# Optimization experiments

Measured on AMD Instinct MI355X. Metric: run time of the kernel, lower is better.

The kernel has to match this reference:

```python
import jax, jax.numpy as jnp
import numpy as np

THRESHOLD = 0.5
NEG_POS_RATIO = 3
VARIANCE = (0.1, 0.2)


def point_form(p):
    # center-form (cx,cy,w,h) -> corner-form (xmin,ymin,xmax,ymax)
    return jnp.concatenate([p[:, :2] - p[:, 2:] / 2, p[:, :2] + p[:, 2:] / 2], axis=-1)


def jaccard(a, b):
    # a: [N,4] corner boxes, b: [P,4] corner boxes -> IoU [N,P]
    lt = jnp.maximum(a[:, None, :2], b[None, :, :2])
    rb = jnp.minimum(a[:, None, 2:], b[None, :, 2:])
    wh = jnp.clip(rb - lt, 0.0)
    inter = wh[..., 0] * wh[..., 1]
    area_a = ((a[:, 2] - a[:, 0]) * (a[:, 3] - a[:, 1]))[:, None]
    area_b = ((b[:, 2] - b[:, 0]) * (b[:, 3] - b[:, 1]))[None, :]
    return inter / (area_a + area_b - inter)


def encode(matched, priors_cf):
    # matched: [P,4] corner GT boxes, priors_cf: [P,4] center-form priors
    g_cxcy = (matched[:, :2] + matched[:, 2:]) / 2 - priors_cf[:, :2]
    g_cxcy = g_cxcy / (VARIANCE[0] * priors_cf[:, 2:])
    g_wh = jnp.log((matched[:, 2:] - matched[:, :2]) / priors_cf[:, 2:]) / VARIANCE[1]
    return jnp.concatenate([g_cxcy, g_wh], axis=-1)  # [P,4]


def match_one(truths, labels, priors_cf):
    # truths: [N,4], labels: [N], priors_cf: [P,4]
    n_obj = truths.shape[0]
    overlaps = jaccard(truths, point_form(priors_cf))          # [N,P]
    best_prior_idx = jnp.argmax(overlaps, axis=1)              # [N] best prior per GT
    best_truth_overlap = jnp.max(overlaps, axis=0)             # [P]
    best_truth_idx = jnp.argmax(overlaps, axis=0)              # [P] best GT per prior
    # ensure every GT keeps its best prior
    best_truth_overlap = best_truth_overlap.at[best_prior_idx].set(2.0)
    best_truth_idx = best_truth_idx.at[best_prior_idx].set(jnp.arange(n_obj))
    matched = truths[best_truth_idx]                           # [P,4]
    conf = jnp.where(best_truth_overlap < THRESHOLD, 0, labels[best_truth_idx] + 1)
    return encode(matched, priors_cf), conf.astype(jnp.int32)


def setup_inputs() -> dict:
    key = jax.random.key(0)
    k1, k2, k3, k4, k5, k6, k7 = jax.random.split(key, 7)
    B, P, C, NOBJ = 64, 24564, 21, 32
    loc_data = jax.random.normal(k1, (B, P, 4), jnp.float32)
    conf_data = jax.random.normal(k2, (B, P, C), jnp.float32)
    p_cxcy = jax.random.uniform(k3, (P, 2), jnp.float32, 0.05, 0.95)
    p_wh = jax.random.uniform(k4, (P, 2), jnp.float32, 0.02, 0.4)
    priors = jnp.concatenate([p_cxcy, p_wh], axis=-1)          # center-form
    t_cxcy = jax.random.uniform(k5, (B, NOBJ, 2), jnp.float32, 0.2, 0.8)
    t_wh = jax.random.uniform(k6, (B, NOBJ, 2), jnp.float32, 0.05, 0.3)
    targets_boxes = jnp.concatenate([t_cxcy - t_wh / 2, t_cxcy + t_wh / 2], axis=-1)
    targets_labels = jax.random.randint(k7, (B, NOBJ), 0, C - 1)  # 0..19, +1 in match
    return {
        "loc_data": loc_data,
        "conf_data": conf_data,
        "priors": priors,
        "targets_boxes": targets_boxes,
        "targets_labels": targets_labels,
    }


def reference(loc_data, conf_data, priors, targets_boxes, targets_labels):
    B, P, C = conf_data.shape
    # targets/priors are detached in the original (.data)
    loc_t, conf_t = jax.vmap(match_one, in_axes=(0, 0, None))(
        jax.lax.stop_gradient(targets_boxes), targets_labels,
        jax.lax.stop_gradient(priors))                          # [B,P,4], [B,P]

    pos = conf_t > 0                                            # [B,P]
    num_pos = jnp.sum(pos, axis=1)                              # [B]

    # localization: smooth L1 on positives, summed
    diff = loc_data - loc_t
    ad = jnp.abs(diff)
    sl1 = jnp.where(ad < 1.0, 0.5 * diff * diff, ad - 0.5)      # [B,P,4]
    loss_l = jnp.sum(sl1 * pos[..., None].astype(sl1.dtype))

    # confidence cross-entropy per prior: lse(x) - x[target]
    lse = jax.nn.logsumexp(conf_data, axis=-1)                  # [B,P]
    gathered = jnp.take_along_axis(conf_data, conf_t[..., None], axis=-1)[..., 0]
    ce_all = lse - gathered                                     # [B,P]

    # hard negative mining: rank negatives by loss, keep top 3*num_pos
    loss_mine = jnp.where(pos, 0.0, ce_all)
    order = jnp.argsort(-loss_mine, axis=1)
    idx_rank = jnp.argsort(order, axis=1)                       # rank of each prior
    num_neg = jnp.clip(NEG_POS_RATIO * num_pos, 0, P - 1)       # [B]
    neg = idx_rank < num_neg[:, None]

    mask = jnp.logical_or(pos, neg)
    loss_c = jnp.sum(ce_all * mask.astype(ce_all.dtype))

    N = jnp.maximum(jnp.sum(num_pos), 1).astype(loss_l.dtype)
    return jnp.stack([loss_l / N, loss_c / N])
```

## Files before the change

kernel.cpp:

```cpp
#include <hip/hip_runtime.h>
#include <stdint.h>

#define THRESH 0.5f
#define VAR0 0.1f
#define VAR1 0.2f
#define SEL_MAXV 32

__global__ __launch_bounds__(256) void fused_kernel(
    const float* __restrict__ loc_data, const float* __restrict__ conf_data,
    const float* __restrict__ priors, const float* __restrict__ tboxes,
    const int* __restrict__ labels,
    unsigned long long* __restrict__ part_best,
    float* __restrict__ loss_mine,
    float* __restrict__ ll_part, float* __restrict__ pc_part,
    int* __restrict__ np_part, unsigned int* __restrict__ done_ctr,
    int P, int C, int NOBJ, int NBLK)
{
#pragma clang fp contract(off)
    extern __shared__ char smem[];
    float* siou = (float*)smem;
    unsigned long long (*sp)[17] =
        (unsigned long long (*)[17])(smem + 16 * 257 * 4);
    float* confs = (float*)smem;
    __shared__ float4 tr[32];
    __shared__ float ta[32];

    const int b = blockIdx.y, bx = blockIdx.x, tid = threadIdx.x;
    const int p = bx * 256 + tid;
    if (b == 0 && bx == 0 && tid == 0) *done_ctr = 0;
    if (tid < NOBJ) {
        float4 t = ((const float4*)tboxes)[(size_t)b * NOBJ + tid];
        tr[tid] = t;
        ta[tid] = (t.z - t.x) * (t.w - t.y);
    }
    __syncthreads();

    const bool valid = (p < P);
    float ax = 0.f, ay = 0.f, bxx = 0.f, byy = 0.f, area_p = 0.f;
    if (valid) {
        float4 pr = ((const float4*)priors)[p];
        ax = pr.x - pr.z * 0.5f;
        ay = pr.y - pr.w * 0.5f;
        bxx = pr.x + pr.z * 0.5f;
        byy = pr.y + pr.w * 0.5f;
        area_p = (bxx - ax) * (byy - ay);
    }

    float bestv = -1.0f;
    int bestn = 0;
    for (int n0 = 0; n0 < NOBJ; n0 += 16) {
        const int jmax = min(16, NOBJ - n0);
        for (int j = 0; j < jmax; ++j) {
            float4 t = tr[n0 + j];
            float iou = -1.0f;
            if (valid) {
                float ltx = fmaxf(t.x, ax), lty = fmaxf(t.y, ay);
                float rbx = fminf(t.z, bxx), rby = fminf(t.w, byy);
                float w = rbx - ltx; if (w < 0.f) w = 0.f;
                float h = rby - lty; if (h < 0.f) h = 0.f;
                float inter = w * h;
                float denom = (ta[n0 + j] + area_p) - inter;
                iou = inter * __builtin_amdgcn_rcpf(denom);
                if (iou > bestv) { bestv = iou; bestn = n0 + j; }
            }
            siou[j * 257 + tid] = iou;
        }
        __syncthreads();
        {
            const int n2 = tid & 15, c = tid >> 4;
            if (n2 < jmax) {
                float bv = -1.0f;
                int bs = 0;
                const int base = n2 * 257 + c * 16;
                for (int j2 = 0; j2 < 16; ++j2) {
                    float v = siou[base + j2];
                    if (v > bv) { bv = v; bs = c * 16 + j2; }
                }
                unsigned long long pk = 0ULL;
                if (bv >= 0.f) {
                    unsigned int pp = (unsigned int)(bx * 256 + bs);
                    pk = (((unsigned long long)__float_as_uint(bv)) << 32) |
                         (unsigned long long)(0xFFFFFFFFu - pp);
                }
                sp[n0 + n2][c] = pk;
            }
        }
        __syncthreads();
    }
    if (tid < NOBJ) {
        unsigned long long best = 0ULL;
        for (int c = 0; c < 16; ++c) {
            unsigned long long v = sp[tid][c];
            if (v > best) best = v;
        }
        part_best[((size_t)b * NBLK + bx) * NOBJ + tid] = best;
    }
    __syncthreads();

    const int p0 = bx * 256;
    const int rows = min(256, P - p0);
    const int nflt = rows * C;
    const float* src = conf_data + ((size_t)b * P + p0) * C;
    if ((((uintptr_t)src) & 15) == 0) {
        const int n4 = nflt >> 2;
        const float4* src4 = (const float4*)src;
        for (int i = tid; i < n4; i += 256) ((float4*)confs)[i] = src4[i];
        for (int i = (n4 << 2) + tid; i < nflt; i += 256) confs[i] = src[i];
    } else {
        for (int i = tid; i < nflt; i += 256) confs[i] = src[i];
    }
    __syncthreads();

    float ll = 0.f, pc = 0.f;
    int np = 0;
    if (tid < rows) {
        const size_t g = (size_t)b * P + p;
        int conf_t = (bestv < THRESH) ? 0 : labels[b * NOBJ + bestn] + 1;

        const float* row = confs + tid * C;
        float s = 0.f;
        for (int j = 0; j < C; ++j) s += __expf(row[j]);
        float ce = __logf(s) - row[conf_t];

        bool pos = (conf_t > 0);
        loss_mine[g] = pos ? 0.f : ce;
        if (pos) {
            np = 1;
            pc = ce;
            float4 t = tr[bestn];
            float4 pr = ((const float4*)priors)[p];
            float gcx = ((t.x + t.z) * 0.5f - pr.x) / (VAR0 * pr.z);
            float gcy = ((t.y + t.w) * 0.5f - pr.y) / (VAR0 * pr.w);
            float gw  = __logf((t.z - t.x) / pr.z) / VAR1;
            float gh  = __logf((t.w - t.y) / pr.w) / VAR1;
            float4 ld = ((const float4*)loc_data)[g];
            float d, a;
            d = ld.x - gcx; a = fabsf(d); ll += (a < 1.f) ? 0.5f * d * d : a - 0.5f;
            d = ld.y - gcy; a = fabsf(d); ll += (a < 1.f) ? 0.5f * d * d : a - 0.5f;
            d = ld.z - gw;  a = fabsf(d); ll += (a < 1.f) ? 0.5f * d * d : a - 0.5f;
            d = ld.w - gh;  a = fabsf(d); ll += (a < 1.f) ? 0.5f * d * d : a - 0.5f;
        }
    }

    for (int off = 32; off; off >>= 1) {
        ll += __shfl_down(ll, off, 64);
        pc += __shfl_down(pc, off, 64);
        np += __shfl_down(np, off, 64);
    }
    __shared__ float sll[4], spc[4];
    __shared__ int snp[4];
    const int lane = tid & 63, wid = tid >> 6;
    if (lane == 0) { sll[wid] = ll; spc[wid] = pc; snp[wid] = np; }
    __syncthreads();
    if (tid == 0) {
        size_t slot = (size_t)b * NBLK + bx;
        ll_part[slot] = sll[0] + sll[1] + sll[2] + sll[3];
        pc_part[slot] = spc[0] + spc[1] + spc[2] + spc[3];
        np_part[slot] = snp[0] + snp[1] + snp[2] + snp[3];
    }
}

__global__ __launch_bounds__(1024) void selectcf_kernel(
    const float* __restrict__ loc_data, const float* __restrict__ conf_data,
    const float* __restrict__ priors, const float* __restrict__ tboxes,
    const int* __restrict__ labels,
    const unsigned long long* __restrict__ part_best,
    float* __restrict__ loss_mine,
    const float* __restrict__ ll_part, const float* __restrict__ pc_part,
    const int* __restrict__ np_part,
    double* __restrict__ neg, double* __restrict__ dll_b,
    double* __restrict__ dpc_b, int* __restrict__ npos_b,
    unsigned int* __restrict__ done_ctr, float* __restrict__ out,
    int P, int C, int NOBJ, int NBLK, int B, int ratio)
{
#pragma clang fp contract(off)
    const int b = blockIdx.x;
    const int tid = threadIdx.x;
    const int lane = tid & 63, wid = tid >> 6;

    __shared__ float4 tr[32];
    __shared__ unsigned long long sp2[32][17];
    __shared__ unsigned long long bb[32];
    __shared__ int2 centry[32];
    __shared__ double sdll[32], sdpc[32];
    __shared__ int cnt_s, snp_s, snp_corr;
    __shared__ unsigned int hist[16][257];
    __shared__ unsigned int merged[256];
    __shared__ unsigned int sh_sel, sh_k;
    __shared__ double sd[16];
    __shared__ unsigned int sc[16];
    __shared__ double negv_s;
    __shared__ int is_last_s;

    if (tid == 0) { cnt_s = 0; snp_s = 0; snp_corr = 0; negv_s = 0.0; }
    if (tid < NOBJ) tr[tid] = ((const float4*)tboxes)[(size_t)b * NOBJ + tid];
    __syncthreads();

    if (tid < NBLK) atomicAdd(&snp_s, np_part[b * NBLK + tid]);

    {
        const int n = tid & 31, c = tid >> 5;
        if (tid < 512 && n < NOBJ) {
            unsigned long long best = 0ULL;
            for (int j = c; j < NBLK; j += 16) {
                unsigned long long v = part_best[((size_t)b * NBLK + j) * NOBJ + n];
                if (v > best) best = v;
            }
            sp2[n][c] = best;
        }
    }
    __syncthreads();
    if (tid < NOBJ) {
        unsigned long long best = 0ULL;
        for (int c = 0; c < 16; ++c) {
            unsigned long long v = sp2[tid][c];
            if (v > best) best = v;
        }
        bb[tid] = best;
    }
    __syncthreads();

    if (tid == 0) {
        int cnt = 0;
        for (int n = 0; n < NOBJ; ++n) {
            int pidx = (int)(0xFFFFFFFFu - (unsigned int)(bb[n] & 0xFFFFFFFFu));
            int f = -1;
            for (int j = 0; j < cnt; ++j)
                if (centry[j].x == pidx) f = j;
            if (f >= 0) centry[f].y = n;
            else { centry[cnt].x = pidx; centry[cnt].y = n; ++cnt; }
        }
        cnt_s = cnt;
    }
    __syncthreads();

    if (tid < cnt_s) {
        const int pidx = centry[tid].x;
        const int n = centry[tid].y;
        float4 pr = ((const float4*)priors)[pidx];
        float ax = pr.x - pr.z * 0.5f;
        float ay = pr.y - pr.w * 0.5f;
        float bxx = pr.x + pr.z * 0.5f;
        float byy = pr.y + pr.w * 0.5f;
        float area_p = (bxx - ax) * (byy - ay);
        float bestv = -1.0f;
        int bestn = 0;
        for (int nn = 0; nn < NOBJ; ++nn) {
            float4 t = tr[nn];
            float ltx = fmaxf(t.x, ax), lty = fmaxf(t.y, ay);
            float rbx = fminf(t.z, bxx), rby = fminf(t.w, byy);
            float w = rbx - ltx; if (w < 0.f) w = 0.f;
            float h = rby - lty; if (h < 0.f) h = 0.f;
            float inter = w * h;
            float att = (t.z - t.x) * (t.w - t.y);
            float denom = (att + area_p) - inter;
            float iou = inter * __builtin_amdgcn_rcpf(denom);
            if (iou > bestv) { bestv = iou; bestn = nn; }
        }
        const float* row = conf_data + ((size_t)b * P + pidx) * C;
        float s = 0.f;
        for (int j = 0; j < C; ++j) s += __expf(row[j]);
        float lse = __logf(s);

        int old_conf = (bestv < THRESH) ? 0 : labels[b * NOBJ + bestn] + 1;
        int new_conf = labels[b * NOBJ + n] + 1;
        bool old_pos = (old_conf > 0);

        double dpc = old_pos ? ((double)row[old_conf] - (double)row[new_conf])
                             : (double)(lse - row[new_conf]);

        const size_t g = (size_t)b * P + pidx;
        float4 ld = ((const float4*)loc_data)[g];
        float sl1_new, sl1_old = 0.f;
        {
            float4 t = tr[n];
            float gcx = ((t.x + t.z) * 0.5f - pr.x) / (VAR0 * pr.z);
            float gcy = ((t.y + t.w) * 0.5f - pr.y) / (VAR0 * pr.w);
            float gw  = __logf((t.z - t.x) / pr.z) / VAR1;
            float gh  = __logf((t.w - t.y) / pr.w) / VAR1;
            float ll = 0.f, d, a;
            d = ld.x - gcx; a = fabsf(d); ll += (a < 1.f) ? 0.5f * d * d : a - 0.5f;
            d = ld.y - gcy; a = fabsf(d); ll += (a < 1.f) ? 0.5f * d * d : a - 0.5f;
            d = ld.z - gw;  a = fabsf(d); ll += (a < 1.f) ? 0.5f * d * d : a - 0.5f;
            d = ld.w - gh;  a = fabsf(d); ll += (a < 1.f) ? 0.5f * d * d : a - 0.5f;
            sl1_new = ll;
        }
        if (old_pos) {
            float4 t = tr[bestn];
            float gcx = ((t.x + t.z) * 0.5f - pr.x) / (VAR0 * pr.z);
            float gcy = ((t.y + t.w) * 0.5f - pr.y) / (VAR0 * pr.w);
            float gw  = __logf((t.z - t.x) / pr.z) / VAR1;
            float gh  = __logf((t.w - t.y) / pr.w) / VAR1;
            float ll = 0.f, d, a;
            d = ld.x - gcx; a = fabsf(d); ll += (a < 1.f) ? 0.5f * d * d : a - 0.5f;
            d = ld.y - gcy; a = fabsf(d); ll += (a < 1.f) ? 0.5f * d * d : a - 0.5f;
            d = ld.z - gw;  a = fabsf(d); ll += (a < 1.f) ? 0.5f * d * d : a - 0.5f;
            d = ld.w - gh;  a = fabsf(d); ll += (a < 1.f) ? 0.5f * d * d : a - 0.5f;
            sl1_old = ll;
        }
        sdll[tid] = (double)sl1_new - (double)sl1_old;
        sdpc[tid] = dpc;
        if (!old_pos) {
            atomicAdd(&snp_corr, 1);
            loss_mine[g] = 0.f;
        }
    }
    __syncthreads();

    int k = ratio * (snp_s + snp_corr);
    if (k > P - 1) k = P - 1;

    if (k > 0) {
        const float* fvals = loss_mine + (size_t)b * P;
        unsigned int vreg[SEL_MAXV];
#pragma unroll
        for (int j = 0; j < SEL_MAXV; ++j) {
            int i = tid + (j << 10);
            vreg[j] = (i < P) ? __float_as_uint(fvals[i]) : 0u;
        }
        unsigned int prefix = 0, mask = 0;
        unsigned int kk = (unsigned int)k;
        for (int shift = 24; shift >= 0; shift -= 8) {
            for (int t = tid; t < 16 * 257; t += 1024) (&hist[0][0])[t] = 0;
            __syncthreads();
            unsigned int* h = hist[wid];
#pragma unroll
            for (int j = 0; j < SEL_MAXV; ++j) {
                int i = tid + (j << 10);
                unsigned int v = vreg[j];
                if (i < P && (v & mask) == prefix)
                    atomicAdd(&h[(v >> shift) & 255u], 1u);
            }
            __syncthreads();
            if (tid < 256) {
                unsigned int s = 0;
                for (int w = 0; w < 16; ++w) s += hist[w][tid];
                merged[tid] = s;
            }
            __syncthreads();
            if (wid == 0) {
                unsigned int h0 = merged[4 * lane], h1 = merged[4 * lane + 1];
                unsigned int h2 = merged[4 * lane + 2], h3 = merged[4 * lane + 3];
                unsigned int s3 = h3, s2 = h2 + s3, s1 = h1 + s2, s0 = h0 + s1;
                unsigned int t = s0;
                unsigned int T = t;
                for (int off = 1; off < 64; off <<= 1) {
                    unsigned int o = __shfl_down(T, off, 64);
                    if (lane + off < 64) T += o;
                }
                unsigned int A = T - t;
                unsigned int S0 = A + s0, S1 = A + s1, S2 = A + s2, S3 = A + s3, S4 = A;
                if (S0 >= kk && S1 < kk) { sh_sel = 4 * lane + 0; sh_k = kk - S1; }
                if (S1 >= kk && S2 < kk) { sh_sel = 4 * lane + 1; sh_k = kk - S2; }
                if (S2 >= kk && S3 < kk) { sh_sel = 4 * lane + 2; sh_k = kk - S3; }
                if (S3 >= kk && S4 < kk) { sh_sel = 4 * lane + 3; sh_k = kk - S4; }
            }
            __syncthreads();
            prefix |= sh_sel << shift;
            mask |= 0xFFu << shift;
            kk = sh_k;
        }
        const float T = __uint_as_float(prefix);

        double sum = 0.0;
        unsigned int cnt = 0;
#pragma unroll
        for (int j = 0; j < SEL_MAXV; ++j) {
            int i = tid + (j << 10);
            if (i < P) {
                float v = __uint_as_float(vreg[j]);
                if (v > T) { sum += (double)v; cnt++; }
            }
        }
        for (int off = 32; off; off >>= 1) {
            sum += __shfl_down(sum, off, 64);
            cnt += __shfl_down(cnt, off, 64);
        }
        if (lane == 0) { sd[wid] = sum; sc[wid] = cnt; }
        __syncthreads();
        if (tid == 0) {
            double S = 0.0;
            unsigned int Cn = 0;
            for (int w = 0; w < 16; ++w) { S += sd[w]; Cn += sc[w]; }
            negv_s = S + (double)((unsigned int)k - Cn) * (double)T;
        }
    }
    __syncthreads();

    if (tid == 0) {
        double DL = 0.0, DP = 0.0;
        for (int j = 0; j < cnt_s; ++j) { DL += sdll[j]; DP += sdpc[j]; }
        neg[b] = negv_s;
        dll_b[b] = DL;
        dpc_b[b] = DP;
        npos_b[b] = snp_s + snp_corr;
        __threadfence();
        unsigned int old = atomicAdd(done_ctr, 1u);
        is_last_s = (old == (unsigned int)B - 1) ? 1 : 0;
    }
    __syncthreads();
    if (!is_last_s) return;
    __threadfence();

    double LL = 0.0, PC = 0.0, NG = 0.0;
    long long NP = 0;
    const int NPART = B * NBLK;
    for (int i = tid; i < NPART; i += 1024) {
        LL += (double)ll_part[i];
        PC += (double)pc_part[i];
    }
    for (int i = tid; i < B; i += 1024) {
        NG += neg[i];
        LL += dll_b[i];
        PC += dpc_b[i];
        NP += (long long)npos_b[i];
    }
    for (int off = 32; off; off >>= 1) {
        LL += __shfl_down(LL, off, 64);
        PC += __shfl_down(PC, off, 64);
        NG += __shfl_down(NG, off, 64);
        NP += __shfl_down(NP, off, 64);
    }
    __shared__ double fll[16], fpc[16], fng[16];
    __shared__ long long fnp[16];
    if (lane == 0) { fll[wid] = LL; fpc[wid] = PC; fng[wid] = NG; fnp[wid] = NP; }
    __syncthreads();
    if (tid == 0) {
        double L = 0.0, Pc = 0.0, Ng = 0.0;
        long long Np = 0;
        for (int w = 0; w < 16; ++w) { L += fll[w]; Pc += fpc[w]; Ng += fng[w]; Np += fnp[w]; }
        if (Np < 1) Np = 1;
        double N = (double)Np;
        out[0] = (float)(L / N);
        out[1] = (float)((Pc + Ng) / N);
    }
}

extern "C" void kernel_launch(void* const* d_in, const int* in_sizes, int n_in,
                              void* d_out, int out_size, void* d_ws, size_t ws_size,
                              hipStream_t stream)
{
    const float* loc_data  = (const float*)d_in[0];
    const float* conf_data = (const float*)d_in[1];
    const float* priors    = (const float*)d_in[2];
    const float* tboxes    = (const float*)d_in[3];
    const int*   tlabels   = (const int*)d_in[4];

    const int P = in_sizes[2] / 4;
    const int B = (int)((long long)in_sizes[0] / ((long long)P * 4));
    const int C = (int)((long long)in_sizes[1] / ((long long)B * P));
    const int NOBJ = in_sizes[4] / B;
    const int NBLK = (P + 255) / 256;

    char* ws = (char*)d_ws;
    size_t off = 0;
    unsigned int* done_ctr = (unsigned int*)(ws + off);  off += 256;
    double* neg = (double*)(ws + off);                   off += (size_t)B * 8;
    off = (off + 255) & ~(size_t)255;
    double* dll_b = (double*)(ws + off);                 off += (size_t)B * 8;
    off = (off + 255) & ~(size_t)255;
    double* dpc_b = (double*)(ws + off);                 off += (size_t)B * 8;
    off = (off + 255) & ~(size_t)255;
    int* npos_b = (int*)(ws + off);                      off += (size_t)B * 4;
    off = (off + 255) & ~(size_t)255;
    float* ll_part = (float*)(ws + off);                 off += (size_t)B * NBLK * 4;
    off = (off + 255) & ~(size_t)255;
    float* pc_part = (float*)(ws + off);                 off += (size_t)B * NBLK * 4;
    off = (off + 255) & ~(size_t)255;
    int* np_part = (int*)(ws + off);                     off += (size_t)B * NBLK * 4;
    off = (off + 255) & ~(size_t)255;
    unsigned long long* part_best = (unsigned long long*)(ws + off);
    off += (size_t)B * NBLK * NOBJ * 8;
    off = (off + 255) & ~(size_t)255;
    float* loss_mine = (float*)(ws + off);

    size_t smem_match = 16 * 257 * 4 + 32 * 17 * 8;
    size_t smem_conf = (size_t)256 * C * 4;
    size_t smem = smem_match > smem_conf ? smem_match : smem_conf;

    dim3 grid(NBLK, B);
    fused_kernel<<<grid, 256, smem, stream>>>(
        loc_data, conf_data, priors, tboxes, tlabels,
        part_best, loss_mine, ll_part, pc_part, np_part, done_ctr,
        P, C, NOBJ, NBLK);
    selectcf_kernel<<<B, 1024, 0, stream>>>(
        loc_data, conf_data, priors, tboxes, tlabels,
        part_best, loss_mine, ll_part, pc_part, np_part,
        neg, dll_b, dpc_b, npos_b, done_ctr, (float*)d_out,
        P, C, NOBJ, NBLK, B, 3);
}
```

Baseline: 306.0 us.

## Load conf rows directly into registers and shrink shared memory in fused kernel

Drops the shared-memory staging of the 256x21 conf tile. Each thread now prefetches its own 21-float row into registers at kernel start, so the load overlaps the IoU matching phase. Shared memory is cut to static arrays (the per-block best packing is split into a float value and a byte index) and launch bounds ask for 8 blocks per CU, aiming for higher occupancy. GT boxes are read from global memory instead of LDS, and the per-thread row loads are strided and unaligned, which may coalesce worse than the old cooperative float4 copy.

Result: faster. 290.9 us (-4.9%).

```diff
diff --git a/kernel.cpp b/kernel.cpp
--- a/kernel.cpp
+++ b/kernel.cpp
@@ -6,7 +6,9 @@
 #define VAR1 0.2f
 #define SEL_MAXV 32
 
-__global__ __launch_bounds__(256) void fused_kernel(
+typedef float f4u __attribute__((ext_vector_type(4), aligned(4)));
+
+__global__ __launch_bounds__(256, 8) void fused_kernel(
     const float* __restrict__ loc_data, const float* __restrict__ conf_data,
     const float* __restrict__ priors, const float* __restrict__ tboxes,
     const int* __restrict__ labels,
@@ -17,20 +19,34 @@
     int P, int C, int NOBJ, int NBLK)
 {
 #pragma clang fp contract(off)
-    extern __shared__ char smem[];
-    float* siou = (float*)smem;
-    unsigned long long (*sp)[17] =
-        (unsigned long long (*)[17])(smem + 16 * 257 * 4);
-    float* confs = (float*)smem;
-    __shared__ float4 tr[32];
+    __shared__ float siou[16 * 257];
+    __shared__ float spv[32][17];
+    __shared__ unsigned char sps[32][20];
     __shared__ float ta[32];
+    __shared__ float sll[4], spc[4];
+    __shared__ int snp[4];
 
     const int b = blockIdx.y, bx = blockIdx.x, tid = threadIdx.x;
-    const int p = bx * 256 + tid;
+    const int p0 = bx * 256;
+    const int p = p0 + tid;
+    const int rows = min(256, P - p0);
     if (b == 0 && bx == 0 && tid == 0) *done_ctr = 0;
+
+    const float4* tb = (const float4*)tboxes + (size_t)b * NOBJ;
+
+    const bool fastC = (C == 21);
+    const float* row = conf_data + ((size_t)b * P + p) * C;
+    f4u q0 = {0,0,0,0}, q1 = {0,0,0,0}, q2 = {0,0,0,0}, q3 = {0,0,0,0},
+        q4 = {0,0,0,0};
+    float q5 = 0.f;
+    if (fastC && tid < rows) {
+        const f4u* r4 = (const f4u*)row;
+        q0 = r4[0]; q1 = r4[1]; q2 = r4[2]; q3 = r4[3]; q4 = r4[4];
+        q5 = row[20];
+    }
+
     if (tid < NOBJ) {
-        float4 t = ((const float4*)tboxes)[(size_t)b * NOBJ + tid];
-        tr[tid] = t;
+        float4 t = tb[tid];
         ta[tid] = (t.z - t.x) * (t.w - t.y);
     }
     __syncthreads();
@@ -50,14 +66,13 @@
     int bestn = 0;
     for (int n0 = 0; n0 < NOBJ; n0 += 16) {
         const int jmax = min(16, NOBJ - n0);
+#pragma unroll 4
         for (int j = 0; j < jmax; ++j) {
-            float4 t = tr[n0 + j];
+            float4 t = tb[n0 + j];
             float iou = -1.0f;
             if (valid) {
-                float ltx = fmaxf(t.x, ax), lty = fmaxf(t.y, ay);
-                float rbx = fminf(t.z, bxx), rby = fminf(t.w, byy);
-                float w = rbx - ltx; if (w < 0.f) w = 0.f;
-                float h = rby - lty; if (h < 0.f) h = 0.f;
+                float w = fminf(t.z, bxx) - fmaxf(t.x, ax); if (w < 0.f) w = 0.f;
+                float h = fminf(t.w, byy) - fmaxf(t.y, ay); if (h < 0.f) h = 0.f;
                 float inter = w * h;
                 float denom = (ta[n0 + j] + area_p) - inter;
                 iou = inter * __builtin_amdgcn_rcpf(denom);
@@ -71,45 +86,33 @@
             if (n2 < jmax) {
                 float bv = -1.0f;
                 int bs = 0;
-                const int base = n2 * 257 + c * 16;
+                const int base = n2 * 257 + c;
                 for (int j2 = 0; j2 < 16; ++j2) {
-                    float v = siou[base + j2];
-                    if (v > bv) { bv = v; bs = c * 16 + j2; }
+                    float v = siou[base + (j2 << 4)];
+                    if (v > bv) { bv = v; bs = (j2 << 4) + c; }
                 }
-                unsigned long long pk = 0ULL;
-                if (bv >= 0.f) {
-                    unsigned int pp = (unsigned int)(bx * 256 + bs);
-                    pk = (((unsigned long long)__float_as_uint(bv)) << 32) |
-                         (unsigned long long)(0xFFFFFFFFu - pp);
-                }
-                sp[n0 + n2][c] = pk;
+                spv[n0 + n2][c] = bv;
+                sps[n0 + n2][c] = (unsigned char)bs;
             }
         }
         __syncthreads();
     }
     if (tid < NOBJ) {
-        unsigned long long best = 0ULL;
-        for (int c = 0; c < 16; ++c) {
-            unsigned long long v = sp[tid][c];
-            if (v > best) best = v;
-        }
-        part_best[((size_t)b * NBLK + bx) * NOBJ + tid] = best;
-    }
-    __syncthreads();
-
-    const int p0 = bx * 256;
-    const int rows = min(256, P - p0);
-    const int nflt = rows * C;
-    const float* src = conf_data + ((size_t)b * P + p0) * C;
-    if ((((uintptr_t)src) & 15) == 0) {
-        const int n4 = nflt >> 2;
-        const float4* src4 = (const float4*)src;
-        for (int i = tid; i < n4; i += 256) ((float4*)confs)[i] = src4[i];
-        for (int i = (n4 << 2) + tid; i < nflt; i += 256) confs[i] = src[i];
-    } else {
-        for (int i = tid; i < nflt; i += 256) confs[i] = src[i];
-    }
-    __syncthreads();
+        float bv = -1.0f;
+        int bs = 0;
+        for (int c2 = 0; c2 < 16; ++c2) {
+            float v = spv[tid][c2];
+            int s2 = (int)sps[tid][c2];
+            if (v > bv || (v == bv && s2 < bs)) { bv = v; bs = s2; }
+        }
+        unsigned long long pk = 0ULL;
+        if (bv >= 0.f) {
+            unsigned int pp = (unsigned int)(p0 + bs);
+            pk = (((unsigned long long)__float_as_uint(bv)) << 32) |
+                 (unsigned long long)(0xFFFFFFFFu - pp);
+        }
+        part_best[((size_t)b * NBLK + bx) * NOBJ + tid] = pk;
+    }
 
     float ll = 0.f, pc = 0.f;
     int np = 0;
@@ -117,17 +120,26 @@
         const size_t g = (size_t)b * P + p;
         int conf_t = (bestv < THRESH) ? 0 : labels[b * NOBJ + bestn] + 1;
 
-        const float* row = confs + tid * C;
-        float s = 0.f;
-        for (int j = 0; j < C; ++j) s += __expf(row[j]);
-        float ce = __logf(s) - row[conf_t];
+        float s;
+        if (fastC) {
+            s  = __expf(q0.x); s += __expf(q0.y); s += __expf(q0.z); s += __expf(q0.w);
+            s += __expf(q1.x); s += __expf(q1.y); s += __expf(q1.z); s += __expf(q1.w);
+            s += __expf(q2.x); s += __expf(q2.y); s += __expf(q2.z); s += __expf(q2.w);
+            s += __expf(q3.x); s += __expf(q3.y); s += __expf(q3.z); s += __expf(q3.w);
+            s += __expf(q4.x); s += __expf(q4.y); s += __expf(q4.z); s += __expf(q4.w);
+            s += __expf(q5);
+        } else {
+            s = 0.f;
+            for (int j = 0; j < C; ++j) s += __expf(row[j]);
+        }
+        float ce = __logf(s) - conf_data[g * (size_t)C + conf_t];
 
         bool pos = (conf_t > 0);
         loss_mine[g] = pos ? 0.f : ce;
         if (pos) {
             np = 1;
             pc = ce;
-            float4 t = tr[bestn];
+            float4 t = tb[bestn];
             float4 pr = ((const float4*)priors)[p];
             float gcx = ((t.x + t.z) * 0.5f - pr.x) / (VAR0 * pr.z);
             float gcy = ((t.y + t.w) * 0.5f - pr.y) / (VAR0 * pr.w);
@@ -147,8 +159,6 @@
         pc += __shfl_down(pc, off, 64);
         np += __shfl_down(np, off, 64);
     }
-    __shared__ float sll[4], spc[4];
-    __shared__ int snp[4];
     const int lane = tid & 63, wid = tid >> 6;
     if (lane == 0) { sll[wid] = ll; spc[wid] = pc; snp[wid] = np; }
     __syncthreads();
@@ -247,10 +257,8 @@
         int bestn = 0;
         for (int nn = 0; nn < NOBJ; ++nn) {
             float4 t = tr[nn];
-            float ltx = fmaxf(t.x, ax), lty = fmaxf(t.y, ay);
-            float rbx = fminf(t.z, bxx), rby = fminf(t.w, byy);
-            float w = rbx - ltx; if (w < 0.f) w = 0.f;
-            float h = rby - lty; if (h < 0.f) h = 0.f;
+            float w = fminf(t.z, bxx) - fmaxf(t.x, ax); if (w < 0.f) w = 0.f;
+            float h = fminf(t.w, byy) - fmaxf(t.y, ay); if (h < 0.f) h = 0.f;
             float inter = w * h;
             float att = (t.z - t.x) * (t.w - t.y);
             float denom = (att + area_p) - inter;
@@ -474,12 +482,8 @@
     off = (off + 255) & ~(size_t)255;
     float* loss_mine = (float*)(ws + off);
 
-    size_t smem_match = 16 * 257 * 4 + 32 * 17 * 8;
-    size_t smem_conf = (size_t)256 * C * 4;
-    size_t smem = smem_match > smem_conf ? smem_match : smem_conf;
-
     dim3 grid(NBLK, B);
-    fused_kernel<<<grid, 256, smem, stream>>>(
+    fused_kernel<<<grid, 256, 0, stream>>>(
         loc_data, conf_data, priors, tboxes, tlabels,
         part_best, loss_mine, ll_part, pc_part, np_part, done_ctr,
         P, C, NOBJ, NBLK);
```
